# Performance work log

Hardware: AMD Instinct MI355X
Metric: run time of the kernel (lower is better)

The kernel has to match this reference:

```python
import jax, jax.numpy as jnp
import numpy as np
from jax import lax

EPS = 1e-08
PAD = 1  # kernel_size // 2 for k=3


def setup_inputs() -> dict:
    key = jax.random.key(0)
    k1, k2, k3, k4 = jax.random.split(key, 4)
    B, Cin, Cout, H, W, K, S = 16, 256, 256, 64, 64, 3, 512
    x = jax.random.normal(k1, (B, Cin, H, W), dtype=jnp.float32)
    style = jax.random.normal(k2, (B, S), dtype=jnp.float32)
    mod_weight = jax.random.normal(k3, (Cin, S), dtype=jnp.float32)
    mod_bias = jnp.zeros((Cin,), dtype=jnp.float32)
    weight = jax.random.normal(k4, (1, Cout, Cin, K, K), dtype=jnp.float32)
    bias = jnp.zeros((1, Cout, 1, 1), dtype=jnp.float32)
    return {"x": x, "style": style, "mod_weight": mod_weight,
            "mod_bias": mod_bias, "weight": weight, "bias": bias}


def reference(x, style, mod_weight, mod_bias, weight, bias):
    # EqualizedLinear modulation (lr_mul = 1.0): s[b, cin]
    s = style @ mod_weight.T + mod_bias  # [B, Cin]
    # per-sample modulated weights: [B, Cout, Cin, K, K]
    w = weight * s[:, None, :, None, None]
    # demodulation: rsqrt of sum over (Cin, K, K)
    demod = lax.rsqrt(jnp.sum(w * w, axis=(2, 3, 4)) + EPS)  # [B, Cout]
    w = w * demod[:, :, None, None, None]

    # per-sample conv2d (groups=B equivalent) via vmap over batch
    def conv_one(xb, wb):
        # xb: [Cin, H, W], wb: [Cout, Cin, K, K]
        return lax.conv_general_dilated(
            xb[None], wb, window_strides=(1, 1),
            padding=[(PAD, PAD), (PAD, PAD)],
            dimension_numbers=("NCHW", "OIHW", "NCHW"))[0]

    out = jax.vmap(conv_one)(x, w)  # [B, Cout, H, W]
    return out + bias
```

## Files before the change

### kernel.cpp

```cpp
#include <hip/hip_runtime.h>

#define EPS 1e-8f
#define THREADS 512

typedef __attribute__((ext_vector_type(8))) short short8;
typedef __attribute__((ext_vector_type(4))) float f32x4;
typedef __attribute__((ext_vector_type(8))) unsigned short u16x8;

static __device__ __forceinline__ unsigned short f2bf(float f) {
  unsigned int u = __float_as_uint(f);
  u += 0x7FFF + ((u >> 16) & 1);
  return (unsigned short)(u >> 16);
}

__global__ void k_prep(const float* __restrict__ style, const float* __restrict__ mw,
                       const float* __restrict__ mb, float* __restrict__ s_out,
                       const float* __restrict__ weight, float* __restrict__ wsq,
                       unsigned short* __restrict__ wbf) {
  __shared__ float sm[2304];
  int t = threadIdx.x;
  if (blockIdx.x < 16) {
    int b = blockIdx.x;
    sm[t]       = style[b*512 + t];
    sm[t + 256] = style[b*512 + 256 + t];
    __syncthreads();
    const float4* row = (const float4*)(mw + (size_t)t*512);
    float acc = 0.f;
#pragma unroll 4
    for (int i = 0; i < 128; ++i) {
      float4 m = row[i];
      acc += m.x*sm[4*i] + m.y*sm[4*i+1] + m.z*sm[4*i+2] + m.w*sm[4*i+3];
    }
    s_out[b*256 + t] = acc + mb[t];
  } else {
    int co = blockIdx.x - 16;
    for (int q = t; q < 576; q += 256)
      *(float4*)&sm[q*4] = *(const float4*)(weight + (size_t)co*2304 + q*4);
    __syncthreads();
    int ci = t;
    int c = ci >> 6, cil = ci & 63;
    int base = ((co*128 + cil*2) ^ ((co & 7) << 4)) >> 1;
    float sum = 0.f;
#pragma unroll
    for (int r = 0; r < 9; ++r) {
      float v = sm[ci*9 + r];
      sum += v*v;
      wbf[(size_t)(c*9 + r)*16384 + base] = f2bf(v);
    }
    wsq[co*256 + ci] = sum;
  }
}

__global__ void k_pad(const float* __restrict__ x, const float* __restrict__ s,
                      unsigned short* __restrict__ xp) {
  int bid = blockIdx.x;
  int b = bid / 66, gh = bid - b*66;
  int t = threadIdx.x;
  size_t rowbase = (size_t)(b*66 + gh) * (66*256);
  u16x8* rp = (u16x8*)(xp + rowbase);
  if (gh == 0 || gh == 65) {
    u16x8 z = (u16x8)0;
    for (int q = t; q < 2112; q += 256) rp[q] = z;
    return;
  }
  int h = gh - 1;
  __shared__ float sl[256];
  __shared__ unsigned short xl[64*256];
  sl[t] = s[b*256 + t];
  __syncthreads();
  int w4 = (t & 15) * 4, o0 = t >> 4;
#pragma unroll
  for (int p = 0; p < 2; ++p) {
    int oct = o0 + p*16;
    u16x8 outv[4];
#pragma unroll
    for (int j = 0; j < 8; ++j) {
      int ci = oct*8 + j;
      float4 v = *(const float4*)(x + ((size_t)(b*256 + ci)*64 + h)*64 + w4);
      float sc = sl[ci];
      outv[0][j] = (short)f2bf(v.x * sc);
      outv[1][j] = (short)f2bf(v.y * sc);
      outv[2][j] = (short)f2bf(v.z * sc);
      outv[3][j] = (short)f2bf(v.w * sc);
    }
#pragma unroll
    for (int k = 0; k < 4; ++k) {
      int w = w4 + k;
      int byte = w*512 + ((oct ^ (w & 31)) << 4);
      *(u16x8*)((char*)xl + byte) = outv[k];
    }
  }
  __syncthreads();
  u16x8 z = (u16x8)0;
  if (t < 32) rp[t] = z;
  else if (t < 64) rp[65*32 + (t - 32)] = z;
  for (int q = t; q < 2048; q += 256) {
    int w2 = q >> 5, slot = q & 31;
    u16x8 v = *(const u16x8*)((char*)xl + w2*512 + ((slot ^ (w2 & 31)) << 4));
    rp[(w2 + 1)*32 + slot] = v;
  }
}

__global__ __launch_bounds__(512, 2)
void k_conv(const unsigned short* __restrict__ xp, const unsigned short* __restrict__ wbf,
            const float* __restrict__ s_buf, const float* __restrict__ wsq,
            const float* __restrict__ bias, float* __restrict__ out) {
  __shared__ unsigned short x_lds[3168*8];
  __shared__ unsigned short w_lds[2*16384];
  __shared__ float s2s[256];
  __shared__ float dms[256];

  const int tid = threadIdx.x;
  const int lane = tid & 63;
  const int wave = tid >> 6;
  const int b = blockIdx.x >> 4;
  const int h0 = (blockIdx.x & 15) * 4;
  const int wm = wave >> 1, wn = wave & 1;
  const int l15 = lane & 15, lk = lane >> 4;

  auto stage_x = [&](int c) {
    int cb = c*64;
#pragma unroll
    for (int it = 0; it < 7; ++it) {
      int q = it*THREADS + tid;
      if (q < 3168) {
        int hw = q >> 3;
        int hl = hw / 66, w = hw - hl*66;
        int slot = (q & 7) ^ (hw & 7);
        const unsigned short* src =
            xp + (size_t)((b*66 + h0 + hl)*66 + w)*256 + cb + slot*8;
        __builtin_amdgcn_global_load_lds(
            (const __attribute__((address_space(1))) void*)src,
            (__attribute__((address_space(3))) void*)&x_lds[(size_t)q*8],
            16, 0, 0);
      }
    }
  };
  auto stage_w = [&](int p) {
    const unsigned short* wsrc = wbf + (size_t)p*16384;
    unsigned short* dst = &w_lds[(p & 1)*16384];
#pragma unroll
    for (int it = 0; it < 4; ++it) {
      int q = it*THREADS + tid;
      __builtin_amdgcn_global_load_lds(
          (const __attribute__((address_space(1))) void*)(wsrc + (size_t)q*8),
          (__attribute__((address_space(3))) void*)&dst[(size_t)q*8],
          16, 0, 0);
    }
  };

  stage_x(0);
  stage_w(0);

  if (tid < 256) { float sv = s_buf[b*256 + tid]; s2s[tid] = sv*sv; }
  asm volatile("s_waitcnt lgkmcnt(0)" ::: "memory");
  __builtin_amdgcn_s_barrier();
  {
    int co = tid >> 1, half = tid & 1;
    const float4* row = (const float4*)(wsq + (size_t)co*256 + half*128);
    const float* sp = &s2s[half*128];
    float a = 0.f;
#pragma unroll 4
    for (int i = 0; i < 32; ++i) {
      float4 q = row[i];
      a += q.x*sp[4*i] + q.y*sp[4*i+1] + q.z*sp[4*i+2] + q.w*sp[4*i+3];
    }
    a += __shfl_xor(a, 1);
    if (half == 0) dms[co] = rsqrtf(a + EPS);
  }

  f32x4 acc[4][8];
#pragma unroll
  for (int m = 0; m < 4; ++m)
#pragma unroll
    for (int f = 0; f < 8; ++f) acc[m][f] = (f32x4)0.f;

  asm volatile("s_waitcnt vmcnt(0) lgkmcnt(0)" ::: "memory");
  __builtin_amdgcn_s_barrier();

  for (int c = 0; c < 4; ++c) {
    for (int r = 0; r < 9; ++r) {
      int p = c*9 + r;
      if (r == 0 && c > 0) stage_x(c);
      if (p < 35) {
        stage_w(p + 1);
        asm volatile("s_waitcnt vmcnt(4)" ::: "memory");
      } else {
        asm volatile("s_waitcnt vmcnt(0)" ::: "memory");
      }
      __builtin_amdgcn_s_barrier();
      __builtin_amdgcn_sched_barrier(0);

      const unsigned short* wbp = &w_lds[(p & 1)*16384];
      int dh = r / 3, dw = r - dh*3;
#pragma unroll
      for (int kh = 0; kh < 2; ++kh) {
        int cio = kh*64 + lk*16;
        short8 a[4], bv[8];
#pragma unroll
        for (int m = 0; m < 4; ++m) {
          int co = wm*64 + m*16 + l15;
          int byte = (co*128 + cio) ^ ((co & 7) << 4);
          a[m] = *(const short8*)((const char*)wbp + byte);
        }
#pragma unroll
        for (int f = 0; f < 8; ++f) {
          int row = (wn*2 + (f >> 2) + dh)*66 + ((f & 3)*16 + l15 + dw);
          int byte = (row*128 + cio) ^ ((row & 7) << 4);
          bv[f] = *(const short8*)((const char*)x_lds + byte);
        }
        __builtin_amdgcn_s_setprio(1);
#pragma unroll
        for (int m = 0; m < 4; ++m)
#pragma unroll
          for (int f = 0; f < 8; ++f)
            acc[m][f] = __builtin_amdgcn_mfma_f32_16x16x32_bf16(a[m], bv[f], acc[m][f], 0, 0, 0);
        __builtin_amdgcn_s_setprio(0);
      }
      __builtin_amdgcn_sched_barrier(0);
      __builtin_amdgcn_s_barrier();
    }
  }

  int colane = (lane >> 4) * 4;
#pragma unroll
  for (int m = 0; m < 4; ++m) {
    int cob = wm*64 + m*16 + colane;
    float4 d4 = *(const float4*)&dms[cob];
    float4 b4 = *(const float4*)&bias[cob];
#pragma unroll
    for (int f = 0; f < 8; ++f) {
      int h = h0 + wn*2 + (f >> 2);
      int wc = (f & 3)*16 + l15;
      float* op = out + ((size_t)(b*256 + cob)*64 + h)*64 + wc;
      op[0]     = acc[m][f][0] * d4.x + b4.x;
      op[4096]  = acc[m][f][1] * d4.y + b4.y;
      op[8192]  = acc[m][f][2] * d4.z + b4.z;
      op[12288] = acc[m][f][3] * d4.w + b4.w;
    }
  }
}

extern "C" void kernel_launch(void* const* d_in, const int* in_sizes, int n_in,
                              void* d_out, int out_size, void* d_ws, size_t ws_size,
                              hipStream_t stream) {
  const float* x      = (const float*)d_in[0];
  const float* style  = (const float*)d_in[1];
  const float* mw     = (const float*)d_in[2];
  const float* mb     = (const float*)d_in[3];
  const float* weight = (const float*)d_in[4];
  const float* bias   = (const float*)d_in[5];
  float* out = (float*)d_out;

  char* ws = (char*)d_ws;
  float* s_buf        = (float*)(ws);
  float* wsq          = (float*)(ws + 16384);
  unsigned short* wbf = (unsigned short*)(ws + 294912);
  unsigned short* xpd = (unsigned short*)(ws + 294912 + 1179648);

  k_prep<<<272, 256, 0, stream>>>(style, mw, mb, s_buf, weight, wsq, wbf);
  k_pad<<<16*66, 256, 0, stream>>>(x, s_buf, xpd);
  k_conv<<<256, 512, 0, stream>>>(xpd, wbf, s_buf, wsq, bias, out);
}
```

Before: 218.0 us.

## Fuse modulation, bf16 conversion and padding into the conv kernel

Drops the separate padding kernel and its padded bf16 intermediate buffer. The conv kernel now loads fp32 x rows directly, scales them by the style vector, converts them to bf16 and writes them into swizzled LDS. It also zeros the halo columns and the edge rows itself. The next channel chunk is prefetched into registers during the last tap of the current chunk, and the explicit vmcnt waits are replaced with __syncthreads. This saves one launch and the write and re-read of the intermediate tensor, at the cost of re-reading halo rows in fp32, higher register pressure and coarser synchronisation.

```diff
diff --git a/kernel.cpp b/kernel.cpp
--- a/kernel.cpp
+++ b/kernel.cpp
@@ -51,62 +51,13 @@
   }
 }
 
-__global__ void k_pad(const float* __restrict__ x, const float* __restrict__ s,
-                      unsigned short* __restrict__ xp) {
-  int bid = blockIdx.x;
-  int b = bid / 66, gh = bid - b*66;
-  int t = threadIdx.x;
-  size_t rowbase = (size_t)(b*66 + gh) * (66*256);
-  u16x8* rp = (u16x8*)(xp + rowbase);
-  if (gh == 0 || gh == 65) {
-    u16x8 z = (u16x8)0;
-    for (int q = t; q < 2112; q += 256) rp[q] = z;
-    return;
-  }
-  int h = gh - 1;
-  __shared__ float sl[256];
-  __shared__ unsigned short xl[64*256];
-  sl[t] = s[b*256 + t];
-  __syncthreads();
-  int w4 = (t & 15) * 4, o0 = t >> 4;
-#pragma unroll
-  for (int p = 0; p < 2; ++p) {
-    int oct = o0 + p*16;
-    u16x8 outv[4];
-#pragma unroll
-    for (int j = 0; j < 8; ++j) {
-      int ci = oct*8 + j;
-      float4 v = *(const float4*)(x + ((size_t)(b*256 + ci)*64 + h)*64 + w4);
-      float sc = sl[ci];
-      outv[0][j] = (short)f2bf(v.x * sc);
-      outv[1][j] = (short)f2bf(v.y * sc);
-      outv[2][j] = (short)f2bf(v.z * sc);
-      outv[3][j] = (short)f2bf(v.w * sc);
-    }
-#pragma unroll
-    for (int k = 0; k < 4; ++k) {
-      int w = w4 + k;
-      int byte = w*512 + ((oct ^ (w & 31)) << 4);
-      *(u16x8*)((char*)xl + byte) = outv[k];
-    }
-  }
-  __syncthreads();
-  u16x8 z = (u16x8)0;
-  if (t < 32) rp[t] = z;
-  else if (t < 64) rp[65*32 + (t - 32)] = z;
-  for (int q = t; q < 2048; q += 256) {
-    int w2 = q >> 5, slot = q & 31;
-    u16x8 v = *(const u16x8*)((char*)xl + w2*512 + ((slot ^ (w2 & 31)) << 4));
-    rp[(w2 + 1)*32 + slot] = v;
-  }
-}
-
 __global__ __launch_bounds__(512, 2)
-void k_conv(const unsigned short* __restrict__ xp, const unsigned short* __restrict__ wbf,
+void k_conv(const float* __restrict__ x, const unsigned short* __restrict__ wbf,
             const float* __restrict__ s_buf, const float* __restrict__ wsq,
             const float* __restrict__ bias, float* __restrict__ out) {
-  __shared__ unsigned short x_lds[3168*8];
+  __shared__ unsigned short x_lds[396*64];
   __shared__ unsigned short w_lds[2*16384];
+  __shared__ float s_lds[256];
   __shared__ float s2s[256];
   __shared__ float dms[256];
 
@@ -117,25 +68,8 @@
   const int h0 = (blockIdx.x & 15) * 4;
   const int wm = wave >> 1, wn = wave & 1;
   const int l15 = lane & 15, lk = lane >> 4;
-
-  auto stage_x = [&](int c) {
-    int cb = c*64;
-#pragma unroll
-    for (int it = 0; it < 7; ++it) {
-      int q = it*THREADS + tid;
-      if (q < 3168) {
-        int hw = q >> 3;
-        int hl = hw / 66, w = hw - hl*66;
-        int slot = (q & 7) ^ (hw & 7);
-        const unsigned short* src =
-            xp + (size_t)((b*66 + h0 + hl)*66 + w)*256 + cb + slot*8;
-        __builtin_amdgcn_global_load_lds(
-            (const __attribute__((address_space(1))) void*)src,
-            (__attribute__((address_space(3))) void*)&x_lds[(size_t)q*8],
-            16, 0, 0);
-      }
-    }
-  };
+  const int oct = (tid >> 4) & 7, w4 = (tid & 15) * 4;
+
   auto stage_w = [&](int p) {
     const unsigned short* wsrc = wbf + (size_t)p*16384;
     unsigned short* dst = &w_lds[(p & 1)*16384];
@@ -148,26 +82,74 @@
           16, 0, 0);
     }
   };
-
-  stage_x(0);
+  auto issue8 = [&](int cc, int hl, float4* v) {
+    int h = h0 + hl - 1;
+    const float* base = x + (((size_t)(b*256 + cc*64 + oct*8))*64 + h)*64 + w4;
+#pragma unroll
+    for (int j = 0; j < 8; ++j) v[j] = *(const float4*)(base + (size_t)j*4096);
+  };
+  auto write8 = [&](int cc, int hl, const float4* v) {
+    u16x8 o0, o1, o2, o3;
+#pragma unroll
+    for (int j = 0; j < 8; ++j) {
+      float sc = s_lds[cc*64 + oct*8 + j];
+      o0[j] = (short)f2bf(v[j].x * sc);
+      o1[j] = (short)f2bf(v[j].y * sc);
+      o2[j] = (short)f2bf(v[j].z * sc);
+      o3[j] = (short)f2bf(v[j].w * sc);
+    }
+    int R0 = hl*66 + w4 + 1;
+    { int R = R0;     *(u16x8*)((char*)x_lds + ((R*128 + oct*16) ^ ((R & 7) << 4))) = o0; }
+    { int R = R0 + 1; *(u16x8*)((char*)x_lds + ((R*128 + oct*16) ^ ((R & 7) << 4))) = o1; }
+    { int R = R0 + 2; *(u16x8*)((char*)x_lds + ((R*128 + oct*16) ^ ((R & 7) << 4))) = o2; }
+    { int R = R0 + 3; *(u16x8*)((char*)x_lds + ((R*128 + oct*16) ^ ((R & 7) << 4))) = o3; }
+  };
+
+  const int hl0 = tid >> 7;
+  const int hl1 = 4 + (tid >> 7);
+  const bool do0 = !(hl0 == 0 && h0 == 0);
+  const bool do1 = (tid < 256) && !(hl1 == 5 && h0 == 60);
+
   stage_w(0);
-
-  if (tid < 256) { float sv = s_buf[b*256 + tid]; s2s[tid] = sv*sv; }
-  asm volatile("s_waitcnt lgkmcnt(0)" ::: "memory");
-  __builtin_amdgcn_s_barrier();
+  if (tid < 256) { float sv = s_buf[b*256 + tid]; s_lds[tid] = sv; s2s[tid] = sv*sv; }
+  if (tid < 96) {
+    int hl = tid >> 4, gw = ((tid >> 3) & 1) * 65, oc = tid & 7;
+    int R = hl*66 + gw;
+    *(u16x8*)((char*)x_lds + ((R*128 + oc*16) ^ ((R & 7) << 4))) = (u16x8)0;
+  }
+  if (h0 == 0) {
+    int oc = tid & 7, gw = 1 + (tid >> 3);
+    int R = gw;
+    *(u16x8*)((char*)x_lds + ((R*128 + oc*16) ^ ((R & 7) << 4))) = (u16x8)0;
+  }
+  if (h0 == 60) {
+    int oc = tid & 7, gw = 1 + (tid >> 3);
+    int R = 5*66 + gw;
+    *(u16x8*)((char*)x_lds + ((R*128 + oc*16) ^ ((R & 7) << 4))) = (u16x8)0;
+  }
+  __syncthreads();
+
   {
-    int co = tid >> 1, half = tid & 1;
-    const float4* row = (const float4*)(wsq + (size_t)co*256 + half*128);
-    const float* sp = &s2s[half*128];
-    float a = 0.f;
+    float4 v0[8], v1[8];
+    if (do0) issue8(0, hl0, v0);
+    if (do1) issue8(0, hl1, v1);
+    {
+      int co = tid >> 1, half = tid & 1;
+      const float4* row = (const float4*)(wsq + (size_t)co*256 + half*128);
+      const float* sp = &s2s[half*128];
+      float a = 0.f;
 #pragma unroll 4
-    for (int i = 0; i < 32; ++i) {
-      float4 q = row[i];
-      a += q.x*sp[4*i] + q.y*sp[4*i+1] + q.z*sp[4*i+2] + q.w*sp[4*i+3];
-    }
-    a += __shfl_xor(a, 1);
-    if (half == 0) dms[co] = rsqrtf(a + EPS);
-  }
+      for (int i = 0; i < 32; ++i) {
+        float4 q = row[i];
+        a += q.x*sp[4*i] + q.y*sp[4*i+1] + q.z*sp[4*i+2] + q.w*sp[4*i+3];
+      }
+      a += __shfl_xor(a, 1);
+      if (half == 0) dms[co] = rsqrtf(a + EPS);
+    }
+    if (do0) write8(0, hl0, v0);
+    if (do1) write8(0, hl1, v1);
+  }
+  __syncthreads();
 
   f32x4 acc[4][8];
 #pragma unroll
@@ -175,22 +157,16 @@
 #pragma unroll
     for (int f = 0; f < 8; ++f) acc[m][f] = (f32x4)0.f;
 
-  asm volatile("s_waitcnt vmcnt(0) lgkmcnt(0)" ::: "memory");
-  __builtin_amdgcn_s_barrier();
-
   for (int c = 0; c < 4; ++c) {
+    float4 v0[8], v1[8];
+#pragma unroll
     for (int r = 0; r < 9; ++r) {
       int p = c*9 + r;
-      if (r == 0 && c > 0) stage_x(c);
-      if (p < 35) {
-        stage_w(p + 1);
-        asm volatile("s_waitcnt vmcnt(4)" ::: "memory");
-      } else {
-        asm volatile("s_waitcnt vmcnt(0)" ::: "memory");
-      }
-      __builtin_amdgcn_s_barrier();
-      __builtin_amdgcn_sched_barrier(0);
-
+      if (r == 8 && c < 3) {
+        if (do0) issue8(c + 1, hl0, v0);
+        if (do1) issue8(c + 1, hl1, v1);
+      }
+      if (p < 35) stage_w(p + 1);
       const unsigned short* wbp = &w_lds[(p & 1)*16384];
       int dh = r / 3, dw = r - dh*3;
 #pragma unroll
@@ -217,8 +193,12 @@
             acc[m][f] = __builtin_amdgcn_mfma_f32_16x16x32_bf16(a[m], bv[f], acc[m][f], 0, 0, 0);
         __builtin_amdgcn_s_setprio(0);
       }
-      __builtin_amdgcn_sched_barrier(0);
-      __builtin_amdgcn_s_barrier();
+      __syncthreads();
+      if (r == 8 && c < 3) {
+        if (do0) write8(c + 1, hl0, v0);
+        if (do1) write8(c + 1, hl1, v1);
+        __syncthreads();
+      }
     }
   }
 
@@ -256,9 +236,7 @@
   float* s_buf        = (float*)(ws);
   float* wsq          = (float*)(ws + 16384);
   unsigned short* wbf = (unsigned short*)(ws + 294912);
-  unsigned short* xpd = (unsigned short*)(ws + 294912 + 1179648);
 
   k_prep<<<272, 256, 0, stream>>>(style, mw, mb, s_buf, weight, wsq, wbf);
-  k_pad<<<16*66, 256, 0, stream>>>(x, s_buf, xpd);
-  k_conv<<<256, 512, 0, stream>>>(xpd, wbf, s_buf, wsq, bias, out);
-}
+  k_conv<<<256, 512, 0, stream>>>(x, wbf, s_buf, wsq, bias, out);
+}
```

Result: slower. 369.9 us (+69.7%).
